# Optimization experiments

Measured on AMD Instinct MI355X. Metric: run time of the kernel, lower is better.

Reference implementation:

```python
import jax, jax.numpy as jnp
import numpy as np

B, T, D = 16, 1024, 256
H, DK = 2, 128          # n_head, d_k = d_v = D // n_head
K = 5                   # conv kernel size
TEMP = float(np.sqrt(D))  # temperature = d_model ** 0.5


def mish(x):
    return x * jnp.tanh(jax.nn.softplus(x))


def setup_inputs() -> dict:
    key = jax.random.key(0)
    ks = jax.random.split(key, 16)
    s = 0.02
    p = lambda k, shp: jax.random.normal(k, shp, dtype=jnp.float32) * s
    inp = {
        'x': jax.random.normal(ks[0], (B, T, D), dtype=jnp.float32),
        'mask': jax.random.randint(ks[1], (B, T), 0, 2).astype(bool),
        # spectral MLP
        'W1': p(ks[2], (D, D)), 'b1': p(ks[3], (D,)),
        'W2': p(ks[4], (D, D)), 'b2': p(ks[5], (D,)),
        # two Conv1dGLU blocks: Conv1d(D -> 2D, k=5), torch layout [out,in,k]
        'cW1': p(ks[6], (2 * D, D, K)), 'cb1': p(ks[7], (2 * D,)),
        'cW2': p(ks[8], (2 * D, D, K)), 'cb2': p(ks[9], (2 * D,)),
        # attention projections (torch Linear: y = x @ W.T + b)
        'Wq': p(ks[10], (D, D)), 'bq': p(ks[11], (D,)),
        'Wk': p(ks[12], (D, D)), 'bk': p(ks[13], (D,)),
        'Wv': p(ks[14], (D, D)), 'bv': p(ks[15], (D,)),
        'Wo': p(jax.random.fold_in(key, 100), (D, D)),
        'bo': p(jax.random.fold_in(key, 101), (D,)),
        # final fc
        'Wf': p(jax.random.fold_in(key, 102), (D, D)),
        'bf': p(jax.random.fold_in(key, 103), (D,)),
    }
    return inp


def conv1d_glu(h, w, b):
    # h: [B, C, T]; w: [2C, C, K]; 'same' padding, GLU gate + residual
    y = jax.lax.conv_general_dilated(h, w, window_strides=(1,), padding=[(K // 2, K // 2)],
                                     dimension_numbers=('NCH', 'OIH', 'NCH'))
    y = y + b[None, :, None]
    a, g = jnp.split(y, 2, axis=1)
    return h + a * jax.nn.sigmoid(g)


def reference(x, mask, W1, b1, W2, b2, cW1, cb1, cW2, cb2,
              Wq, bq, Wk, bk, Wv, bv, Wo, bo, Wf, bf):
    # spectral: Linear + Mish (dropout is identity at inference)
    h = mish(x @ W1.T + b1)
    h = mish(h @ W2.T + b2)
    # temporal: two Conv1dGLU residual blocks over [B, C, T]
    h = h.transpose(0, 2, 1)
    h = conv1d_glu(h, cW1, cb1)
    h = conv1d_glu(h, cW2, cb2)
    h = h.transpose(0, 2, 1)
    # zero out padded frames
    h = jnp.where(mask[:, :, None], 0.0, h)
    residual = h
    # multi-head self-attention; mask hides padded keys
    q = (h @ Wq.T + bq).reshape(B, T, H, DK)
    k = (h @ Wk.T + bk).reshape(B, T, H, DK)
    v = (h @ Wv.T + bv).reshape(B, T, H, DK)
    attn = jnp.einsum('bqhd,bkhd->bhqk', q, k) / TEMP
    attn = jnp.where(mask[:, None, None, :], -jnp.inf, attn)
    attn = jax.nn.softmax(attn, axis=-1)
    out = jnp.einsum('bhqk,bkhd->bqhd', attn, v).reshape(B, T, D)
    h = out @ Wo.T + bo + residual
    # final projection + masked temporal average pool
    y = h @ Wf.T + bf
    len_ = (~mask).sum(axis=1, keepdims=True).astype(y.dtype)  # [B,1]
    y = jnp.where(mask[:, :, None], 0.0, y)
    w = y.sum(axis=1) / len_
    return w
```

## Files before the change

kernel.cpp:

```cpp
#include <hip/hip_runtime.h>
#include <hip/hip_bf16.h>
#include <math.h>


#define DEV __device__ __forceinline__

static constexpr int B_ = 16, T_ = 1024, D_ = 256;
static constexpr int N_ = B_ * T_;

typedef __attribute__((ext_vector_type(8))) short bf16x8;
typedef __attribute__((ext_vector_type(16))) float floatx16;

DEV float sigmoidf_(float x) { return 1.f / (1.f + __expf(-x)); }
DEV float mishf_(float x) {
  float u = __expf(fminf(x, 30.f));
  float t = u * (u + 2.f);
  return x * (t / (t + 2.f));
}
DEV ushort f2bf_(float x) {
  __hip_bfloat16 h = __float2bfloat16(x);
  return *(ushort*)&h;
}

__global__ __launch_bounds__(256) void prep_all_kernel(
    const unsigned* __restrict__ mraw,
    const float* __restrict__ W1, const float* __restrict__ W2,
    const float* __restrict__ Wq, const float* __restrict__ Wk,
    const float* __restrict__ Wv, const float* __restrict__ Wo,
    const float* __restrict__ cW1, const float* __restrict__ cW2,
    ushort* __restrict__ w1, ushort* __restrict__ w2,
    ushort* __restrict__ wqkv, ushort* __restrict__ wo,
    ushort* __restrict__ WtF1, ushort* __restrict__ WtF2,
    float* __restrict__ fmask, ushort* __restrict__ QE,
    ushort* __restrict__ KF, float* __restrict__ pooled) {
  int bid = blockIdx.x, tid = threadIdx.x;
  if (bid < 384) {
    int i = bid * 256 + tid;
    int widx = i >> 14, r = i & 16383;
    const float* src;
    ushort* dst;
    switch (widx) {
      case 0: src = W1; dst = w1; break;
      case 1: src = W2; dst = w2; break;
      case 2: src = Wq; dst = wqkv; break;
      case 3: src = Wk; dst = wqkv + 65536; break;
      case 4: src = Wv; dst = wqkv + 131072; break;
      default: src = Wo; dst = wo; break;
    }
    float4 v = ((const float4*)src)[r];
    ushort4 u;
    u.x = f2bf_(v.x); u.y = f2bf_(v.y); u.z = f2bf_(v.z); u.w = f2bf_(v.w);
    ((ushort4*)dst)[r] = u;
  } else if (bid < 5504) {
    int idx = (bid - 384) * 256 + tid;
    const float* cw = (idx < 655360) ? cW1 : cW2;
    ushort* dst = (idx < 655360) ? WtF1 : WtF2;
    int i = (idx < 655360) ? idx : idx - 655360;
    int j = i & 7, half = (i >> 3) & 1, m31 = (i >> 4) & 31;
    int frag = i >> 9;
    int ks = frag & 1, c = (frag >> 1) & 7, tap = (frag >> 4) % 5,
        cot = frag / 80;
    int co = cot * 32 + m31;
    int cin = c * 32 + ks * 16 + half * 8 + j;
    dst[i] = f2bf_(cw[(size_t)(co * 256 + cin) * 5 + tap]);
  } else {
    int isByte = 0, isFloat = 0;
    for (int i = 0; i < 16; ++i) {
      unsigned v = mraw[tid * 16 + i];
      if (v == 0x3F800000u) isFloat = 1;
      else if (v > 1u) isByte = 1;
    }
    __shared__ int sByte, sFloat;
    if (tid == 0) { sByte = 0; sFloat = 0; }
    __syncthreads();
    if (isByte) atomicOr(&sByte, 1);
    if (isFloat) atomicOr(&sFloat, 1);
    __syncthreads();
    int mode = sFloat ? 2 : (sByte ? 1 : 0);
    int mb = bid - 5504;
    int id = mb * 256 + tid;
    int bh = id >> 10, t = id & 1023, b = bh >> 1;
    int gidx = b * 1024 + t;
    unsigned mv;
    if (mode == 1) mv = ((const unsigned char*)mraw)[gidx];
    else           mv = mraw[gidx];
    float fm = (mv != 0u) ? 1.f : 0.f;
    if ((bh & 1) == 0) fmask[gidx] = fm;
    if (mb < 16) pooled[mb * 256 + tid] = 0.f;
    size_t qb = (size_t)id * 144 + 128;
    QE[qb] = f2bf_(1.f);
#pragma unroll
    for (int j = 1; j < 16; ++j) QE[qb + j] = 0;
    size_t kb = ((size_t)(bh * 32 + (t >> 5)) * 9 + 8) * 512 + (t & 31) * 16;
    KF[kb] = (fm != 0.f) ? f2bf_(-60000.f) : (ushort)0;
#pragma unroll
    for (int j = 1; j < 16; ++j) KF[kb + j] = 0;
  }
}

template <int ACT, int RESID, int OMODE, int AF32>
__global__ __launch_bounds__(256, 4) void gemm_mfma_kernel(
    const void* __restrict__ Av, const ushort* __restrict__ W16,
    const float* __restrict__ bias, const float* __restrict__ resid,
    const float* __restrict__ fmask,
    float* __restrict__ outf, ushort* __restrict__ outb) {
  __shared__ __align__(16) ushort As[2][32 * 40];
  int tid = threadIdx.x;
  int w = tid >> 6, lane = tid & 63;
  int m31 = lane & 31, half = lane >> 5;
  int n0 = blockIdx.x * 32;
  int col = blockIdx.y * 128 + w * 32 + m31;
  const ushort* A16 = (const ushort*)Av;
  const float* A32 = (const float*)Av;

  floatx16 acc;
#pragma unroll
  for (int i = 0; i < 16; ++i) acc[i] = 0.f;

  {
    int row = tid >> 3, part = tid & 7;
    if (AF32) {
      float4 v = *(const float4*)&A32[(size_t)(n0 + row) * 256 + part * 4];
      ushort4 u;
      u.x = f2bf_(v.x); u.y = f2bf_(v.y); u.z = f2bf_(v.z); u.w = f2bf_(v.w);
      *(ushort4*)&As[0][row * 40 + part * 4] = u;
    } else {
      *(uint2*)&As[0][row * 40 + part * 4] =
          *(const uint2*)&A16[(size_t)(n0 + row) * 256 + part * 4];
    }
  }
  bf16x8 bn[2];
#pragma unroll
  for (int ks = 0; ks < 2; ++ks)
    bn[ks] = *(const bf16x8*)&W16[(size_t)col * 256 + ks * 16 + half * 8];

  for (int c = 0; c < 8; ++c) {
    __syncthreads();
    if (c < 7) {
      int k0 = (c + 1) * 32;
      int row = tid >> 3, part = tid & 7;
      if (AF32) {
        float4 v = *(const float4*)&A32[(size_t)(n0 + row) * 256 + k0 + part * 4];
        ushort4 u;
        u.x = f2bf_(v.x); u.y = f2bf_(v.y); u.z = f2bf_(v.z); u.w = f2bf_(v.w);
        *(ushort4*)&As[(c + 1) & 1][row * 40 + part * 4] = u;
      } else {
        *(uint2*)&As[(c + 1) & 1][row * 40 + part * 4] =
            *(const uint2*)&A16[(size_t)(n0 + row) * 256 + k0 + part * 4];
      }
    }
    bf16x8 bc[2] = {bn[0], bn[1]};
    if (c < 7) {
      int k0 = (c + 1) * 32;
#pragma unroll
      for (int ks = 0; ks < 2; ++ks)
        bn[ks] = *(const bf16x8*)&W16[(size_t)col * 256 + k0 + ks * 16 + half * 8];
    }
    const ushort* ab = As[c & 1];
#pragma unroll
    for (int ks = 0; ks < 2; ++ks) {
      bf16x8 af = *(const bf16x8*)&ab[m31 * 40 + ks * 16 + half * 8];
      acc = __builtin_amdgcn_mfma_f32_32x32x16_bf16(af, bc[ks], acc, 0, 0, 0);
    }
  }
  float bv = bias[col];
  if (OMODE == 3) {
    int b = n0 >> 10;
    float psum = 0.f;
#pragma unroll
    for (int reg = 0; reg < 16; ++reg) {
      int row = n0 + (reg & 3) + 8 * (reg >> 2) + 4 * half;
      float keep = (fmask[row] == 0.f) ? 1.f : 0.f;
      psum += keep * (acc[reg] + bv + resid[(size_t)row * 256 + col]);
    }
    atomicAdd(&outf[b * 256 + col], psum);
    return;
  }
#pragma unroll
  for (int reg = 0; reg < 16; ++reg) {
    int row = n0 + (reg & 3) + 8 * (reg >> 2) + 4 * half;
    float v = acc[reg] + bv;
    if (ACT == 1) v = mishf_(v);
    if (RESID) v += resid[(size_t)row * 256 + col];
    if (OMODE == 0) {
      outf[(size_t)row * 256 + col] = v;
    } else if (OMODE == 1) {
      outb[(size_t)row * 256 + col] = f2bf_(v);
    } else {
      outf[(size_t)row * 256 + col] = v;
      outb[(size_t)row * 256 + col] = f2bf_(v);
    }
  }
}

__global__ __launch_bounds__(256, 4) void qkv_mfma_kernel(
    const ushort* __restrict__ A16, const ushort* __restrict__ wqkv,
    const float* __restrict__ bq, const float* __restrict__ bk,
    const float* __restrict__ bv,
    ushort* __restrict__ QE, ushort* __restrict__ KF, ushort* __restrict__ VF) {
  __shared__ __align__(16) ushort As[2][32 * 40];
  int tid = threadIdx.x;
  int w = tid >> 6, lane = tid & 63;
  int m31 = lane & 31, half = lane >> 5;
  int n0 = blockIdx.x * 32;
  int by = blockIdx.z;
  const ushort* W16 = wqkv + (size_t)by * 65536;
  const float* bias = (by == 0) ? bq : (by == 1) ? bk : bv;
  int col = blockIdx.y * 128 + w * 32 + m31;

  floatx16 acc;
#pragma unroll
  for (int i = 0; i < 16; ++i) acc[i] = 0.f;

  {
    int row = tid >> 3, part = tid & 7;
    *(uint2*)&As[0][row * 40 + part * 4] =
        *(const uint2*)&A16[(size_t)(n0 + row) * 256 + part * 4];
  }
  bf16x8 bn[2];
#pragma unroll
  for (int ks = 0; ks < 2; ++ks)
    bn[ks] = *(const bf16x8*)&W16[(size_t)col * 256 + ks * 16 + half * 8];

  for (int c = 0; c < 8; ++c) {
    __syncthreads();
    if (c < 7) {
      int k0 = (c + 1) * 32;
      int row = tid >> 3, part = tid & 7;
      *(uint2*)&As[(c + 1) & 1][row * 40 + part * 4] =
          *(const uint2*)&A16[(size_t)(n0 + row) * 256 + k0 + part * 4];
    }
    bf16x8 bc[2] = {bn[0], bn[1]};
    if (c < 7) {
      int k0 = (c + 1) * 32;
#pragma unroll
      for (int ks = 0; ks < 2; ++ks)
        bn[ks] = *(const bf16x8*)&W16[(size_t)col * 256 + k0 + ks * 16 + half * 8];
    }
    const ushort* ab = As[c & 1];
#pragma unroll
    for (int ks = 0; ks < 2; ++ks) {
      bf16x8 af = *(const bf16x8*)&ab[m31 * 40 + ks * 16 + half * 8];
      acc = __builtin_amdgcn_mfma_f32_32x32x16_bf16(af, bc[ks], acc, 0, 0, 0);
    }
  }
  int b = n0 >> 10;
  float bvv = bias[col];
  int h = col >> 7, d127 = col & 127;
  int bh = b * 2 + h;
  if (by == 2) {
    int ctv = d127 >> 5, m31v = d127 & 31;
#pragma unroll
    for (int rg = 0; rg < 4; ++rg) {
      int t0 = (n0 & 1023) + 8 * rg + 4 * half;
      ushort4 u;
      u.x = f2bf_(acc[rg * 4 + 0] + bvv);
      u.y = f2bf_(acc[rg * 4 + 1] + bvv);
      u.z = f2bf_(acc[rg * 4 + 2] + bvv);
      u.w = f2bf_(acc[rg * 4 + 3] + bvv);
      size_t addr = ((size_t)(bh * 16 + (t0 >> 6)) * 16 +
                     ((t0 >> 4) & 3) * 4 + ctv) * 512 +
                    m31v * 16 + ((t0 >> 3) & 1) * 8 + (t0 & 7);
      *(ushort4*)&VF[addr] = u;
    }
  } else {
#pragma unroll
    for (int reg = 0; reg < 16; ++reg) {
      int t = (n0 & 1023) + (reg & 3) + 8 * (reg >> 2) + 4 * half;
      float v = acc[reg] + bvv;
      if (by == 0) {
        QE[((size_t)(bh * 1024 + t)) * 144 + d127] = f2bf_(v * 0.0625f);
      } else {
        size_t addr = ((size_t)(bh * 32 + (t >> 5)) * 9 + (d127 >> 4)) * 512 +
                      (t & 31) * 16 + ((d127 >> 3) & 1) * 8 + (d127 & 7);
        KF[addr] = f2bf_(v);
      }
    }
  }
}

template <int DO_MASK>
__global__ __launch_bounds__(256, 3) void conv_mfma_kernel(
    const ushort* __restrict__ H16, const float* __restrict__ Hf,
    const ushort* __restrict__ WtF, const float* __restrict__ cb,
    const float* __restrict__ fmask, float* __restrict__ outf,
    ushort* __restrict__ outb) {
  __shared__ __align__(16) ushort As[2][68 * 40];
  int tid = threadIdx.x;
  int w = tid >> 6, lane = tid & 63;
  int m31 = lane & 31, half = lane >> 5;
  int wr = w >> 1, wc = w & 1;
  int n0 = blockIdx.x * 64;
  int cg = blockIdx.y;
  int tbase = n0 & 1023;
  int acol = cg * 64 + wc * 32;
  int cotA = cg * 2 + wc, cotG = 8 + cg * 2 + wc;

  floatx16 acc[2];
#pragma unroll
  for (int ct = 0; ct < 2; ++ct)
#pragma unroll
    for (int i = 0; i < 16; ++i) acc[ct][i] = 0.f;

  for (int i = tid; i < 544; i += 256) {
    int row = i >> 3, part = i & 7;
    int t = tbase + row - 2;
    uint2 v = make_uint2(0u, 0u);
    if ((unsigned)t < 1024u)
      v = *(const uint2*)&H16[(size_t)(n0 + row - 2) * 256 + part * 4];
    *(uint2*)&As[0][row * 40 + part * 4] = v;
  }
  bf16x8 bn[2][2];
#pragma unroll
  for (int ks = 0; ks < 2; ++ks) {
    bn[ks][0] = *(const bf16x8*)&WtF[(size_t)(((cotA * 5 + 0) * 8 + 0) * 2 + ks) * 512 +
                                     m31 * 16 + half * 8];
    bn[ks][1] = *(const bf16x8*)&WtF[(size_t)(((cotG * 5 + 0) * 8 + 0) * 2 + ks) * 512 +
                                     m31 * 16 + half * 8];
  }

  for (int c = 0; c < 8; ++c) {
    __syncthreads();
    if (c < 7) {
      int k0 = (c + 1) * 32;
      for (int i = tid; i < 544; i += 256) {
        int row = i >> 3, part = i & 7;
        int t = tbase + row - 2;
        uint2 v = make_uint2(0u, 0u);
        if ((unsigned)t < 1024u)
          v = *(const uint2*)&H16[(size_t)(n0 + row - 2) * 256 + k0 + part * 4];
        *(uint2*)&As[(c + 1) & 1][row * 40 + part * 4] = v;
      }
    }
    const ushort* ab = As[c & 1];
#pragma unroll
    for (int tap = 0; tap < 5; ++tap) {
      bf16x8 bc[2][2];
#pragma unroll
      for (int ks = 0; ks < 2; ++ks)
#pragma unroll
        for (int ct = 0; ct < 2; ++ct) bc[ks][ct] = bn[ks][ct];
      int pc = c, pt = tap + 1;
      if (pt == 5) { pc = c + 1; pt = 0; }
      if (pc < 8) {
#pragma unroll
        for (int ks = 0; ks < 2; ++ks) {
          bn[ks][0] = *(const bf16x8*)&WtF[
              (size_t)(((cotA * 5 + pt) * 8 + pc) * 2 + ks) * 512 + m31 * 16 + half * 8];
          bn[ks][1] = *(const bf16x8*)&WtF[
              (size_t)(((cotG * 5 + pt) * 8 + pc) * 2 + ks) * 512 + m31 * 16 + half * 8];
        }
      }
#pragma unroll
      for (int ks = 0; ks < 2; ++ks) {
        bf16x8 af = *(const bf16x8*)&ab[(wr * 32 + m31 + tap) * 40 +
                                        ks * 16 + half * 8];
#pragma unroll
        for (int ct = 0; ct < 2; ++ct)
          acc[ct] = __builtin_amdgcn_mfma_f32_32x32x16_bf16(
              af, bc[ks][ct], acc[ct], 0, 0, 0);
      }
    }
  }
  int col = acol + m31;
  float ba = cb[col], bg = cb[256 + col];
#pragma unroll
  for (int reg = 0; reg < 16; ++reg) {
    int brow = wr * 32 + (reg & 3) + 8 * (reg >> 2) + 4 * half;
    int grow = n0 + brow;
    float a = acc[0][reg] + ba;
    float g = acc[1][reg] + bg;
    float v = Hf[(size_t)grow * 256 + col] + a * sigmoidf_(g);
    if (DO_MASK) {
      if (fmask[grow] != 0.f) v = 0.f;
    }
    outf[(size_t)grow * 256 + col] = v;
    outb[(size_t)grow * 256 + col] = f2bf_(v);
  }
}

__global__ __launch_bounds__(256, 2) void attn_mfma2_kernel(
    const ushort* __restrict__ QE, const ushort* __restrict__ KF,
    const ushort* __restrict__ VF, ushort* __restrict__ O) {
  __shared__ float Op[2][128][33];
  __shared__ float Ml[2][2][32];
  int tid = threadIdx.x;
  int w = tid >> 6, lane = tid & 63;
  int m31 = lane & 31, half = lane >> 5;
  int qt = w & 1, kh = w >> 1;
  int bh = blockIdx.x;
  int q0 = blockIdx.y * 64 + qt * 32;
  int lpos = m31 * 16 + half * 8;

  bf16x8 qe[9];
  {
    size_t qrow = ((size_t)(bh * 1024 + q0 + m31)) * 144;
#pragma unroll
    for (int c = 0; c < 9; ++c)
      qe[c] = *(const bf16x8*)&QE[qrow + c * 16 + half * 8];
  }
  floatx16 oacc[4];
#pragma unroll
  for (int ct = 0; ct < 4; ++ct)
#pragma unroll
    for (int i = 0; i < 16; ++i) oacc[ct][i] = 0.f;
  float mi = -1e30f, li = 0.f;

  for (int it = 0; it < 8; ++it) {
    int ktb = kh * 512 + it * 64;
    int kfrag = (bh * 32 + (ktb >> 5)) * 9;
    int vtile = (bh * 16 + (ktb >> 6)) * 16;
    floatx16 s0, s1;
#pragma unroll
    for (int i = 0; i < 16; ++i) { s0[i] = 0.f; s1[i] = 0.f; }
#pragma unroll
    for (int c = 0; c < 9; ++c) {
      bf16x8 kf0 = *(const bf16x8*)&KF[(size_t)(kfrag + c) * 512 + lpos];
      bf16x8 kf1 = *(const bf16x8*)&KF[(size_t)(kfrag + 9 + c) * 512 + lpos];
      s0 = __builtin_amdgcn_mfma_f32_32x32x16_bf16(kf0, qe[c], s0, 0, 0, 0);
      s1 = __builtin_amdgcn_mfma_f32_32x32x16_bf16(kf1, qe[c], s1, 0, 0, 0);
    }
    bf16x8 vfr[2][4];
#pragma unroll
    for (int s2 = 0; s2 < 2; ++s2)
#pragma unroll
      for (int ct = 0; ct < 4; ++ct)
        vfr[s2][ct] = *(const bf16x8*)&VF[(size_t)(vtile + s2 * 4 + ct) * 512 + lpos];
    float mloc = s0[0];
#pragma unroll
    for (int r = 1; r < 16; ++r) mloc = fmaxf(mloc, s0[r]);
#pragma unroll
    for (int r = 0; r < 16; ++r) mloc = fmaxf(mloc, s1[r]);
    float mt = fmaxf(mloc, __shfl_xor(mloc, 32));
    float mnew = fmaxf(mi, mt);
    float alpha = __expf(mi - mnew);
    bool dead = (mnew <= -3.0e4f);
    float sum = 0.f;
#pragma unroll
    for (int r = 0; r < 16; ++r) {
      float v0 = dead ? 0.f : __expf(s0[r] - mnew);
      float v1 = dead ? 0.f : __expf(s1[r] - mnew);
      s0[r] = v0; s1[r] = v1;
      sum += v0 + v1;
    }
    sum += __shfl_xor(sum, 32);
    li = li * alpha + sum;
    mi = mnew;
#pragma unroll
    for (int ct = 0; ct < 4; ++ct)
#pragma unroll
      for (int i = 0; i < 16; ++i) oacc[ct][i] *= alpha;
    bf16x8 pf[4];
#pragma unroll
    for (int sub = 0; sub < 2; ++sub) {
      float tx[16];
#pragma unroll
      for (int r = 0; r < 16; ++r)
        tx[r] = __shfl_xor(sub == 0 ? s0[r] : s1[r], 32);
#pragma unroll
      for (int s = 0; s < 2; ++s) {
        union { bf16x8 v; ushort u[8]; } pk;
#pragma unroll
        for (int j = 0; j < 8; ++j) {
          int base = s * 8;
          float own = (sub == 0) ? s0[base + j] : s1[base + j];
          float lo = (j < 4) ? own : tx[base + j - 4];
          float hi = (j < 4) ? tx[base + 4 + j] : own;
          pk.u[j] = f2bf_(half ? hi : lo);
        }
        pf[sub * 2 + s] = pk.v;
      }
    }
#pragma unroll
    for (int s2 = 0; s2 < 4; ++s2)
#pragma unroll
      for (int ct = 0; ct < 4; ++ct) {
        bf16x8 vf = (s2 < 2) ? vfr[s2][ct]
                  : *(const bf16x8*)&VF[(size_t)(vtile + s2 * 4 + ct) * 512 + lpos];
        oacc[ct] = __builtin_amdgcn_mfma_f32_32x32x16_bf16(
            vf, pf[s2], oacc[ct], 0, 0, 0);
      }
  }
  if (kh == 1) {
#pragma unroll
    for (int ct = 0; ct < 4; ++ct)
#pragma unroll
      for (int r = 0; r < 16; ++r) {
        int dv = ct * 32 + (r & 3) + 8 * (r >> 2) + 4 * half;
        Op[qt][dv][m31] = oacc[ct][r];
      }
    if (half == 0) { Ml[qt][0][m31] = mi; Ml[qt][1][m31] = li; }
  }
  __syncthreads();
  if (kh == 0) {
    float mB = Ml[qt][0][m31], lB = Ml[qt][1][m31];
    float m = fmaxf(mi, mB);
    float aA = __expf(mi - m), aB = __expf(mB - m);
    float l = li * aA + lB * aB;
    float inv = (l > 0.f) ? 1.f / l : 0.f;
    int b = bh >> 1, h = bh & 1;
    size_t rowbase = (size_t)(b * 1024 + q0 + m31) * 256 + h * 128;
#pragma unroll
    for (int ct = 0; ct < 4; ++ct)
#pragma unroll
      for (int rg = 0; rg < 4; ++rg) {
        int dv0 = ct * 32 + 8 * rg + 4 * half;
        ushort4 u;
        u.x = f2bf_((oacc[ct][rg * 4 + 0] * aA + Op[qt][dv0 + 0][m31] * aB) * inv);
        u.y = f2bf_((oacc[ct][rg * 4 + 1] * aA + Op[qt][dv0 + 1][m31] * aB) * inv);
        u.z = f2bf_((oacc[ct][rg * 4 + 2] * aA + Op[qt][dv0 + 2][m31] * aB) * inv);
        u.w = f2bf_((oacc[ct][rg * 4 + 3] * aA + Op[qt][dv0 + 3][m31] * aB) * inv);
        *(ushort4*)&O[rowbase + dv0] = u;
      }
  }
}

__global__ __launch_bounds__(256) void final_kernel(
    const float* __restrict__ pooled, const float* __restrict__ fmask,
    const float* __restrict__ Wf, const float* __restrict__ bf,
    float* __restrict__ out) {
  int b = blockIdx.x, j = threadIdx.x;
  __shared__ __align__(16) float p[256];
  __shared__ float red[256];
  p[j] = pooled[b * 256 + j];
  float c = 0.f;
  for (int i = 0; i < 4; ++i)
    c += (fmask[b * 1024 + i * 256 + j] == 0.f) ? 1.f : 0.f;
  red[j] = c;
  __syncthreads();
  for (int st = 128; st > 0; st >>= 1) {
    if (j < st) red[j] += red[j + st];
    __syncthreads();
  }
  float len = red[0];
  const float* wrow = Wf + (size_t)j * 256;
  float acc = 0.f;
  for (int d4 = 0; d4 < 64; ++d4) {
    float4 wv = ((const float4*)wrow)[d4];
    float4 pv = ((const float4*)p)[d4];
    acc += wv.x * pv.x + wv.y * pv.y + wv.z * pv.z + wv.w * pv.w;
  }
  float inv = (len > 0.f) ? 1.f / len : 0.f;
  out[b * 256 + j] = acc * inv + bf[j];
}

extern "C" void kernel_launch(void* const* d_in, const int* in_sizes, int n_in,
                              void* d_out, int out_size, void* d_ws, size_t ws_size,
                              hipStream_t stream) {
  const float* x      = (const float*)d_in[0];
  const unsigned* msk = (const unsigned*)d_in[1];
  const float* W1 = (const float*)d_in[2];
  const float* b1 = (const float*)d_in[3];
  const float* W2 = (const float*)d_in[4];
  const float* b2 = (const float*)d_in[5];
  const float* cW1 = (const float*)d_in[6];
  const float* cb1 = (const float*)d_in[7];
  const float* cW2 = (const float*)d_in[8];
  const float* cb2 = (const float*)d_in[9];
  const float* Wq = (const float*)d_in[10];
  const float* bq = (const float*)d_in[11];
  const float* Wk = (const float*)d_in[12];
  const float* bk = (const float*)d_in[13];
  const float* Wv = (const float*)d_in[14];
  const float* bv = (const float*)d_in[15];
  const float* Wo = (const float*)d_in[16];
  const float* bo = (const float*)d_in[17];
  const float* Wf = (const float*)d_in[18];
  const float* bf = (const float*)d_in[19];
  float* out = (float*)d_out;

  float* ws = (float*)d_ws;
  size_t ND = (size_t)N_ * D_;
  float* F0      = ws;
  float* F1      = F0 + ND;
  float* fmask   = F1 + ND;
  float* pooled  = fmask + N_;
  ushort* G0 = (ushort*)(pooled + 16 * 256);
  ushort* G1 = G0 + ND;
  ushort* QE = G1 + ND;
  ushort* KF = QE + (size_t)32 * 1024 * 144;
  ushort* VF = KF + (size_t)32 * 32 * 9 * 512;
  ushort* w1_16 = VF + (size_t)32 * 16 * 16 * 512;
  ushort* w2_16 = w1_16 + 65536;
  ushort* wo_16 = w2_16 + 65536;
  ushort* wqkv  = wo_16 + 65536;
  ushort* WtF1  = wqkv + 3 * 65536;
  ushort* WtF2  = WtF1 + 655360;

  dim3 blk(256);
  prep_all_kernel<<<dim3(5632), blk, 0, stream>>>(
      msk, W1, W2, Wq, Wk, Wv, Wo, cW1, cW2,
      w1_16, w2_16, wqkv, wo_16, WtF1, WtF2, fmask, QE, KF, pooled);
  gemm_mfma_kernel<1, 0, 1, 1><<<dim3(512, 2), blk, 0, stream>>>(
      x, w1_16, b1, nullptr, nullptr, nullptr, G1);
  gemm_mfma_kernel<1, 0, 2, 0><<<dim3(512, 2), blk, 0, stream>>>(
      G1, w2_16, b2, nullptr, nullptr, F0, G0);
  conv_mfma_kernel<0><<<dim3(256, 4), blk, 0, stream>>>(
      G0, F0, WtF1, cb1, fmask, F1, G1);
  conv_mfma_kernel<1><<<dim3(256, 4), blk, 0, stream>>>(
      G1, F1, WtF2, cb2, fmask, F0, G0);
  qkv_mfma_kernel<<<dim3(512, 2, 3), blk, 0, stream>>>(
      G0, wqkv, bq, bk, bv, QE, KF, VF);
  attn_mfma2_kernel<<<dim3(32, 16), blk, 0, stream>>>(QE, KF, VF, G1);
  gemm_mfma_kernel<0, 1, 3, 0><<<dim3(512, 2), blk, 0, stream>>>(
      G1, wo_16, bo, F0, fmask, pooled, nullptr);
  final_kernel<<<dim3(16), blk, 0, stream>>>(pooled, fmask, Wf, bf, out);
}
```

Before: 323.7 us.

## Store Q in MFMA fragment layout via LDS staging, vectorize conv weight prep

Q is now written in the same tiled fragment layout as K, staged through a per-wave LDS buffer so both Q and K stores become 16-byte coalesced writes instead of scattered 2-byte ones. The attention kernel reads Q fragments contiguously, drops the V-fragment prefetch registers, and raises launch bounds to 3 blocks per CU for more occupancy. The conv weight repack writes 8 bf16 values per thread with one vector store, cutting the prep grid size. Risks: lost V prefetch may expose load latency in attention, and the new LDS staging adds shared memory use and a write/read pass per wave.

```diff
diff --git a/kernel.cpp b/kernel.cpp
--- a/kernel.cpp
+++ b/kernel.cpp
@@ -31,7 +31,7 @@
     ushort* __restrict__ w1, ushort* __restrict__ w2,
     ushort* __restrict__ wqkv, ushort* __restrict__ wo,
     ushort* __restrict__ WtF1, ushort* __restrict__ WtF2,
-    float* __restrict__ fmask, ushort* __restrict__ QE,
+    float* __restrict__ fmask, ushort* __restrict__ QF,
     ushort* __restrict__ KF, float* __restrict__ pooled) {
   int bid = blockIdx.x, tid = threadIdx.x;
   if (bid < 384) {
@@ -51,18 +51,23 @@
     ushort4 u;
     u.x = f2bf_(v.x); u.y = f2bf_(v.y); u.z = f2bf_(v.z); u.w = f2bf_(v.w);
     ((ushort4*)dst)[r] = u;
-  } else if (bid < 5504) {
+  } else if (bid < 1024) {
     int idx = (bid - 384) * 256 + tid;
-    const float* cw = (idx < 655360) ? cW1 : cW2;
-    ushort* dst = (idx < 655360) ? WtF1 : WtF2;
-    int i = (idx < 655360) ? idx : idx - 655360;
-    int j = i & 7, half = (i >> 3) & 1, m31 = (i >> 4) & 31;
+    const float* cw = (idx < 81920) ? cW1 : cW2;
+    ushort* dst = (idx < 81920) ? WtF1 : WtF2;
+    int i8 = (idx < 81920) ? idx : idx - 81920;
+    int i = i8 * 8;
+    int half = (i >> 3) & 1, m31 = (i >> 4) & 31;
     int frag = i >> 9;
     int ks = frag & 1, c = (frag >> 1) & 7, tap = (frag >> 4) % 5,
         cot = frag / 80;
     int co = cot * 32 + m31;
-    int cin = c * 32 + ks * 16 + half * 8 + j;
-    dst[i] = f2bf_(cw[(size_t)(co * 256 + cin) * 5 + tap]);
+    int cin0 = c * 32 + ks * 16 + half * 8;
+    ushort u[8];
+#pragma unroll
+    for (int j = 0; j < 8; ++j)
+      u[j] = f2bf_(cw[(size_t)(co * 256 + cin0 + j) * 5 + tap]);
+    *(uint4*)&dst[i] = *(uint4*)u;
   } else {
     int isByte = 0, isFloat = 0;
     for (int i = 0; i < 16; ++i) {
@@ -77,7 +82,7 @@
     if (isFloat) atomicOr(&sFloat, 1);
     __syncthreads();
     int mode = sFloat ? 2 : (sByte ? 1 : 0);
-    int mb = bid - 5504;
+    int mb = bid - 1024;
     int id = mb * 256 + tid;
     int bh = id >> 10, t = id & 1023, b = bh >> 1;
     int gidx = b * 1024 + t;
@@ -87,10 +92,10 @@
     float fm = (mv != 0u) ? 1.f : 0.f;
     if ((bh & 1) == 0) fmask[gidx] = fm;
     if (mb < 16) pooled[mb * 256 + tid] = 0.f;
-    size_t qb = (size_t)id * 144 + 128;
-    QE[qb] = f2bf_(1.f);
-#pragma unroll
-    for (int j = 1; j < 16; ++j) QE[qb + j] = 0;
+    size_t qb = ((size_t)(bh * 32 + (t >> 5)) * 9 + 8) * 512 + (t & 31) * 16;
+    QF[qb] = f2bf_(1.f);
+#pragma unroll
+    for (int j = 1; j < 16; ++j) QF[qb + j] = 0;
     size_t kb = ((size_t)(bh * 32 + (t >> 5)) * 9 + 8) * 512 + (t & 31) * 16;
     KF[kb] = (fm != 0.f) ? f2bf_(-60000.f) : (ushort)0;
 #pragma unroll
@@ -197,8 +202,9 @@
     const ushort* __restrict__ A16, const ushort* __restrict__ wqkv,
     const float* __restrict__ bq, const float* __restrict__ bk,
     const float* __restrict__ bv,
-    ushort* __restrict__ QE, ushort* __restrict__ KF, ushort* __restrict__ VF) {
+    ushort* __restrict__ QF, ushort* __restrict__ KF, ushort* __restrict__ VF) {
   __shared__ __align__(16) ushort As[2][32 * 40];
+  __shared__ __align__(16) ushort Tw[4][32 * 40];
   int tid = threadIdx.x;
   int w = tid >> 6, lane = tid & 63;
   int m31 = lane & 31, half = lane >> 5;
@@ -264,17 +270,22 @@
       *(ushort4*)&VF[addr] = u;
     }
   } else {
+    float scale = (by == 0) ? 0.0625f : 1.f;
+    ushort* tw = &Tw[w][0];
 #pragma unroll
     for (int reg = 0; reg < 16; ++reg) {
-      int t = (n0 & 1023) + (reg & 3) + 8 * (reg >> 2) + 4 * half;
-      float v = acc[reg] + bvv;
-      if (by == 0) {
-        QE[((size_t)(bh * 1024 + t)) * 144 + d127] = f2bf_(v * 0.0625f);
-      } else {
-        size_t addr = ((size_t)(bh * 32 + (t >> 5)) * 9 + (d127 >> 4)) * 512 +
-                      (t & 31) * 16 + ((d127 >> 3) & 1) * 8 + (d127 & 7);
-        KF[addr] = f2bf_(v);
-      }
+      int brow = (reg & 3) + 8 * (reg >> 2) + 4 * half;
+      tw[brow * 40 + m31] = f2bf_((acc[reg] + bvv) * scale);
+    }
+    ushort* dst = (by == 0) ? QF : KF;
+    int tile9 = (bh * 32 + ((n0 & 1023) >> 5)) * 9;
+    int c0 = (d127 & 127) >> 4;
+    c0 = ((blockIdx.y * 128 + w * 32) & 127) >> 4;
+    int tr = lane >> 1, hb = lane & 1;
+#pragma unroll
+    for (int cc = 0; cc < 2; ++cc) {
+      uint4 v = *(const uint4*)&tw[tr * 40 + cc * 16 + hb * 8];
+      *(uint4*)&dst[(size_t)(tile9 + c0 + cc) * 512 + lane * 8] = v;
     }
   }
 }
@@ -379,8 +390,8 @@
   }
 }
 
-__global__ __launch_bounds__(256, 2) void attn_mfma2_kernel(
-    const ushort* __restrict__ QE, const ushort* __restrict__ KF,
+__global__ __launch_bounds__(256, 3) void attn_mfma2_kernel(
+    const ushort* __restrict__ QF, const ushort* __restrict__ KF,
     const ushort* __restrict__ VF, ushort* __restrict__ O) {
   __shared__ float Op[2][128][33];
   __shared__ float Ml[2][2][32];
@@ -394,10 +405,10 @@
 
   bf16x8 qe[9];
   {
-    size_t qrow = ((size_t)(bh * 1024 + q0 + m31)) * 144;
+    int qtile9 = (bh * 32 + (q0 >> 5)) * 9;
 #pragma unroll
     for (int c = 0; c < 9; ++c)
-      qe[c] = *(const bf16x8*)&QE[qrow + c * 16 + half * 8];
+      qe[c] = *(const bf16x8*)&QF[(size_t)(qtile9 + c) * 512 + lpos];
   }
   floatx16 oacc[4];
 #pragma unroll
@@ -420,12 +431,6 @@
       s0 = __builtin_amdgcn_mfma_f32_32x32x16_bf16(kf0, qe[c], s0, 0, 0, 0);
       s1 = __builtin_amdgcn_mfma_f32_32x32x16_bf16(kf1, qe[c], s1, 0, 0, 0);
     }
-    bf16x8 vfr[2][4];
-#pragma unroll
-    for (int s2 = 0; s2 < 2; ++s2)
-#pragma unroll
-      for (int ct = 0; ct < 4; ++ct)
-        vfr[s2][ct] = *(const bf16x8*)&VF[(size_t)(vtile + s2 * 4 + ct) * 512 + lpos];
     float mloc = s0[0];
 #pragma unroll
     for (int r = 1; r < 16; ++r) mloc = fmaxf(mloc, s0[r]);
@@ -475,8 +480,7 @@
     for (int s2 = 0; s2 < 4; ++s2)
 #pragma unroll
       for (int ct = 0; ct < 4; ++ct) {
-        bf16x8 vf = (s2 < 2) ? vfr[s2][ct]
-                  : *(const bf16x8*)&VF[(size_t)(vtile + s2 * 4 + ct) * 512 + lpos];
+        bf16x8 vf = *(const bf16x8*)&VF[(size_t)(vtile + s2 * 4 + ct) * 512 + lpos];
         oacc[ct] = __builtin_amdgcn_mfma_f32_32x32x16_bf16(
             vf, pf[s2], oacc[ct], 0, 0, 0);
       }
@@ -577,8 +581,8 @@
   float* pooled  = fmask + N_;
   ushort* G0 = (ushort*)(pooled + 16 * 256);
   ushort* G1 = G0 + ND;
-  ushort* QE = G1 + ND;
-  ushort* KF = QE + (size_t)32 * 1024 * 144;
+  ushort* QF = G1 + ND;
+  ushort* KF = QF + (size_t)32 * 32 * 9 * 512;
   ushort* VF = KF + (size_t)32 * 32 * 9 * 512;
   ushort* w1_16 = VF + (size_t)32 * 16 * 16 * 512;
   ushort* w2_16 = w1_16 + 65536;
@@ -588,9 +592,9 @@
   ushort* WtF2  = WtF1 + 655360;
 
   dim3 blk(256);
-  prep_all_kernel<<<dim3(5632), blk, 0, stream>>>(
+  prep_all_kernel<<<dim3(1152), blk, 0, stream>>>(
       msk, W1, W2, Wq, Wk, Wv, Wo, cW1, cW2,
-      w1_16, w2_16, wqkv, wo_16, WtF1, WtF2, fmask, QE, KF, pooled);
+      w1_16, w2_16, wqkv, wo_16, WtF1, WtF2, fmask, QF, KF, pooled);
   gemm_mfma_kernel<1, 0, 1, 1><<<dim3(512, 2), blk, 0, stream>>>(
       x, w1_16, b1, nullptr, nullptr, nullptr, G1);
   gemm_mfma_kernel<1, 0, 2, 0><<<dim3(512, 2), blk, 0, stream>>>(
@@ -600,8 +604,8 @@
   conv_mfma_kernel<1><<<dim3(256, 4), blk, 0, stream>>>(
       G1, F1, WtF2, cb2, fmask, F0, G0);
   qkv_mfma_kernel<<<dim3(512, 2, 3), blk, 0, stream>>>(
-      G0, wqkv, bq, bk, bv, QE, KF, VF);
-  attn_mfma2_kernel<<<dim3(32, 16), blk, 0, stream>>>(QE, KF, VF, G1);
+      G0, wqkv, bq, bk, bv, QF, KF, VF);
+  attn_mfma2_kernel<<<dim3(32, 16), blk, 0, stream>>>(QF, KF, VF, G1);
   gemm_mfma_kernel<0, 1, 3, 0><<<dim3(512, 2), blk, 0, stream>>>(
       G1, wo_16, bo, F0, fmask, pooled, nullptr);
   final_kernel<<<dim3(16), blk, 0, stream>>>(pooled, fmask, Wf, bf, out);
```

New measurement: 322.0 us. No clear change (-0.5%).
